# Optimization experiments

Measured on AMD Instinct MI355X. Metric: run time of the kernel, lower is better.

The kernel has to match this reference:

```python
import jax, jax.numpy as jnp
import numpy as np

N_ROUTINGS = 3


def squash(v, axis=-1):
    sn = jnp.sum(jnp.square(v), axis=axis, keepdims=True)
    return (jnp.sqrt(sn) / (1.0 + sn)) * v


def setup_inputs() -> dict:
    key = jax.random.key(0)
    k1, k2 = jax.random.split(key)
    B, R, C, n_in, d_in = 16, 14, 14, 64, 16
    n_caps, caps_dim = 10, 16
    inputs = jax.random.normal(k1, (B, R, C, n_in, d_in), dtype=jnp.float32)
    W = jax.random.normal(k2, (n_caps, n_in, d_in, caps_dim), dtype=jnp.float32) * 0.1
    return {"inputs": inputs, "W": W}


def reference(inputs, W):
    # inputs: [B,R,C,i,e], W: [n,i,e,o] -> res (u_hat): [B,R,C,n,i,o]
    res = jnp.einsum('brcie,nieo->brcnio', inputs, W)
    n_in = inputs.shape[3]
    # softmax of zeros over last axis -> uniform 1/n_in
    b = jnp.full(res.shape[:-1], 1.0 / n_in, dtype=res.dtype)  # [B,R,C,n,i]
    for _ in range(N_ROUTINGS - 1):
        v = squash(jnp.sum(b[..., None] * res, axis=-2))  # [B,R,C,n,o]
        b = b + jnp.sum(res * v[..., None, :], axis=-1)   # agreement
    out = squash(jnp.sum(b[..., None] * res, axis=-2))
    return out  # [B,R,C,n_caps,caps_dim]
```

## Files before the change

### kernel.cpp

```cpp
#include <hip/hip_runtime.h>
#include <hip/hip_bf16.h>

typedef __attribute__((ext_vector_type(4))) float f32x4;
typedef __attribute__((ext_vector_type(8))) short s16x8;

#define GLOBAL_AS __attribute__((address_space(1)))
#define LDS_AS    __attribute__((address_space(3)))
#define QPB 8


template<int CTRL>
__device__ __forceinline__ float dpp_add(float x) {
    int v = __builtin_amdgcn_update_dpp(0, __float_as_int(x), CTRL, 0xF, 0xF, true);
    return x + __int_as_float(v);
}
template<int CTRL>
__device__ __forceinline__ float dpp_movf(float x) {
    return __int_as_float(__builtin_amdgcn_update_dpp(0, __float_as_int(x), CTRL, 0xF, 0xF, true));
}

__global__ __launch_bounds__(256, 3) void caps_kernel(
    const float* __restrict__ inp,
    const float* __restrict__ W,
    float* __restrict__ out)
{
    const int tid = threadIdx.x;
    const int w   = tid >> 6;
    const int l   = tid & 63;
    const int n   = blockIdx.x / 98;
    const int qg  = blockIdx.x % 98;
    const int q0  = qg * QPB;

    extern __shared__ __align__(16) char smem[];
    char*  res_s = smem;
    float* W_s   = (float*)(smem + 16384);

    const int i4 = l >> 2;
    const int oq = l & 3;
    const int i_ = w * 16 + i4;
    const int col = l & 15;
    const int kg  = l >> 4;

    f32x4 raw[4], rawn[4];
#pragma unroll
    for (int p = 0; p < 4; ++p)
        raw[p] = *(const f32x4*)(inp + (size_t)q0 * 4096 + p * 1024 + w * 256 + l * 4);

    const float* Wn = W + (size_t)n * 16384;
    f32x4 wrot[16];
    for (int k = 0; k < 4; ++k) {
#pragma unroll
        for (int k2 = 0; k2 < 4; ++k2) {
            int d  = k2 * 256 + tid;
            int ir = d >> 6;
            int cd = d & 63;
            int c  = cd ^ (ir & 7);
            __builtin_amdgcn_global_load_lds(
                (const GLOBAL_AS unsigned int*)(Wn + (k * 1024 + ir * 64 + c) * 4),
                (LDS_AS unsigned int*)((char*)W_s + d * 16), 16, 0, 0);
        }
        __syncthreads();
        if (w == k) {
#pragma unroll
            for (int r = 0; r < 4; ++r) {
                int c = (oq + r) & 3;
#pragma unroll
                for (int kk = 0; kk < 4; ++kk) {
                    int e = c * 4 + kk;
                    wrot[r * 4 + kk] =
                        *(const f32x4*)(W_s + i4 * 256 + (((e * 4 + oq) ^ (i4 & 7)) << 2));
                }
            }
        }
        __syncthreads();
    }

    s16x8 ones;
#pragma unroll
    for (int j = 0; j < 8; ++j) ones[j] = (short)0x3F80;

#pragma unroll 2
    for (int t = 0; t < QPB; ++t) {
        const int q = q0 + t;
        char* rbuf = res_s + (t & 1) * 8192;

        if (t + 1 < QPB) {
#pragma unroll
            for (int p = 0; p < 4; ++p)
                rawn[p] = *(const f32x4*)(inp + (size_t)(q + 1) * 4096 + p * 1024 + w * 256 + l * 4);
        }

#pragma unroll
        for (int p = 0; p < 4; ++p) {
            f32x4 a = raw[p];
            f32x4 acc = (f32x4)0.0f;
#pragma unroll
            for (int kk = 0; kk < 4; ++kk) acc += a[kk] * wrot[kk];
            f32x4 b1;
#pragma unroll
            for (int kk = 0; kk < 4; ++kk) b1[kk] = dpp_movf<0x39>(a[kk]);
#pragma unroll
            for (int kk = 0; kk < 4; ++kk) acc += b1[kk] * wrot[4 + kk];
            f32x4 b2;
#pragma unroll
            for (int kk = 0; kk < 4; ++kk) b2[kk] = dpp_movf<0x4E>(a[kk]);
#pragma unroll
            for (int kk = 0; kk < 4; ++kk) acc += b2[kk] * wrot[8 + kk];
            f32x4 b3;
#pragma unroll
            for (int kk = 0; kk < 4; ++kk) b3[kk] = dpp_movf<0x93>(a[kk]);
#pragma unroll
            for (int kk = 0; kk < 4; ++kk) acc += b3[kk] * wrot[12 + kk];

#pragma unroll
            for (int dd = 0; dd < 4; ++dd) {
                int o = oq * 4 + dd;
                __hip_bfloat16 bb = __float2bfloat16(acc[dd]);
                int byte = p * 2048 + o * 128 + (((i_ >> 3) ^ (o & 7)) << 4) + (i_ & 7) * 2;
                *(unsigned short*)(rbuf + byte) = *(unsigned short*)&bb;
            }
        }

        asm volatile("s_waitcnt lgkmcnt(0)" ::: "memory");
        __builtin_amdgcn_s_barrier();
        asm volatile("" ::: "memory");
        __builtin_amdgcn_sched_barrier(0);

        s16x8 fr0 = *(const s16x8*)(rbuf + w * 2048 + col * 128 + (((kg + 0) ^ (col & 7)) << 4));
        s16x8 fr1 = *(const s16x8*)(rbuf + w * 2048 + col * 128 + (((kg + 4) ^ (col & 7)) << 4));

        f32x4 G  = (f32x4)0.0f;
        f32x4 C2 = (f32x4)0.0f;
        G  = __builtin_amdgcn_mfma_f32_16x16x32_bf16(fr0, fr0, G, 0, 0, 0);
        G  = __builtin_amdgcn_mfma_f32_16x16x32_bf16(fr1, fr1, G, 0, 0, 0);
        C2 = __builtin_amdgcn_mfma_f32_16x16x32_bf16(ones, fr0, C2, 0, 0, 0);
        C2 = __builtin_amdgcn_mfma_f32_16x16x32_bf16(ones, fr1, C2, 0, 0, 0);

        float s = C2[0] * (1.0f / 64.0f);

#pragma unroll
        for (int it = 0; it < 2; ++it) {
            float sn = s * s;
            sn = dpp_add<0xB1>(sn);
            sn = dpp_add<0x4E>(sn);
            sn = dpp_add<0x124>(sn);
            sn = dpp_add<0x128>(sn);
            float scale = sqrtf(sn) / (1.0f + sn);
            float v = scale * s;
            float v0 = __shfl(v, kg * 4 + 0);
            float v1 = __shfl(v, kg * 4 + 1);
            float v2 = __shfl(v, kg * 4 + 2);
            float v3 = __shfl(v, kg * 4 + 3);
            float acc = G[0] * v0 + G[1] * v1 + G[2] * v2 + G[3] * v3;
            acc += __shfl_xor(acc, 16);
            acc += __shfl_xor(acc, 32);
            s += acc;
        }

        float sn = s * s;
        sn = dpp_add<0xB1>(sn);
        sn = dpp_add<0x4E>(sn);
        sn = dpp_add<0x124>(sn);
        sn = dpp_add<0x128>(sn);
        float scale = sqrtf(sn) / (1.0f + sn);
        float v = scale * s;

        if (l < 16)
            out[((size_t)(q * 4 + w) * 10 + n) * 16 + col] = v;

        if (t + 1 < QPB) {
#pragma unroll
            for (int p = 0; p < 4; ++p) raw[p] = rawn[p];
        }
    }
}

extern "C" void kernel_launch(void* const* d_in, const int* in_sizes, int n_in,
                              void* d_out, int out_size, void* d_ws, size_t ws_size,
                              hipStream_t stream) {
    const float* inp = (const float*)d_in[0];
    const float* W   = (const float*)d_in[1];
    float* out = (float*)d_out;

    dim3 grid(980), block(256);
    hipLaunchKernelGGL(caps_kernel, grid, block, 32768, stream, inp, W, out);
}
```

Measured before the change: 36.39 us.

## Load W directly from global, halve positions per block, raise occupancy

After: 34.42 us. 5.4% less time.

```diff
diff --git a/kernel.cpp b/kernel.cpp
--- a/kernel.cpp
+++ b/kernel.cpp
@@ -4,9 +4,7 @@
 typedef __attribute__((ext_vector_type(4))) float f32x4;
 typedef __attribute__((ext_vector_type(8))) short s16x8;
 
-#define GLOBAL_AS __attribute__((address_space(1)))
-#define LDS_AS    __attribute__((address_space(3)))
-#define QPB 8
+#define QPB 4
 
 
 template<int CTRL>
@@ -19,7 +17,7 @@
     return __int_as_float(__builtin_amdgcn_update_dpp(0, __float_as_int(x), CTRL, 0xF, 0xF, true));
 }
 
-__global__ __launch_bounds__(256, 3) void caps_kernel(
+__global__ __launch_bounds__(256, 4) void caps_kernel(
     const float* __restrict__ inp,
     const float* __restrict__ W,
     float* __restrict__ out)
@@ -27,13 +25,12 @@
     const int tid = threadIdx.x;
     const int w   = tid >> 6;
     const int l   = tid & 63;
-    const int n   = blockIdx.x / 98;
-    const int qg  = blockIdx.x % 98;
+    const int n   = blockIdx.x / 196;
+    const int qg  = blockIdx.x % 196;
     const int q0  = qg * QPB;
 
     extern __shared__ __align__(16) char smem[];
-    char*  res_s = smem;
-    float* W_s   = (float*)(smem + 16384);
+    char* res_s = smem;
 
     const int i4 = l >> 2;
     const int oq = l & 3;
@@ -41,54 +38,28 @@
     const int col = l & 15;
     const int kg  = l >> 4;
 
-    f32x4 raw[4], rawn[4];
+    const float* wb = W + (size_t)n * 16384 + i_ * 256 + oq * 4;
+    f32x4 wrot[16];
 #pragma unroll
-    for (int p = 0; p < 4; ++p)
-        raw[p] = *(const f32x4*)(inp + (size_t)q0 * 4096 + p * 1024 + w * 256 + l * 4);
-
-    const float* Wn = W + (size_t)n * 16384;
-    f32x4 wrot[16];
-    for (int k = 0; k < 4; ++k) {
+    for (int r = 0; r < 4; ++r) {
+        int c = (oq + r) & 3;
 #pragma unroll
-        for (int k2 = 0; k2 < 4; ++k2) {
-            int d  = k2 * 256 + tid;
-            int ir = d >> 6;
-            int cd = d & 63;
-            int c  = cd ^ (ir & 7);
-            __builtin_amdgcn_global_load_lds(
-                (const GLOBAL_AS unsigned int*)(Wn + (k * 1024 + ir * 64 + c) * 4),
-                (LDS_AS unsigned int*)((char*)W_s + d * 16), 16, 0, 0);
-        }
-        __syncthreads();
-        if (w == k) {
-#pragma unroll
-            for (int r = 0; r < 4; ++r) {
-                int c = (oq + r) & 3;
-#pragma unroll
-                for (int kk = 0; kk < 4; ++kk) {
-                    int e = c * 4 + kk;
-                    wrot[r * 4 + kk] =
-                        *(const f32x4*)(W_s + i4 * 256 + (((e * 4 + oq) ^ (i4 & 7)) << 2));
-                }
-            }
-        }
-        __syncthreads();
+        for (int kk = 0; kk < 4; ++kk)
+            wrot[r * 4 + kk] = *(const f32x4*)(wb + (c * 4 + kk) * 16);
     }
 
     s16x8 ones;
 #pragma unroll
     for (int j = 0; j < 8; ++j) ones[j] = (short)0x3F80;
 
-#pragma unroll 2
     for (int t = 0; t < QPB; ++t) {
         const int q = q0 + t;
         char* rbuf = res_s + (t & 1) * 8192;
 
-        if (t + 1 < QPB) {
+        f32x4 raw[4];
 #pragma unroll
-            for (int p = 0; p < 4; ++p)
-                rawn[p] = *(const f32x4*)(inp + (size_t)(q + 1) * 4096 + p * 1024 + w * 256 + l * 4);
-        }
+        for (int p = 0; p < 4; ++p)
+            raw[p] = *(const f32x4*)(inp + (size_t)q * 4096 + p * 1024 + w * 256 + l * 4);
 
 #pragma unroll
         for (int p = 0; p < 4; ++p) {
@@ -167,11 +138,6 @@
 
         if (l < 16)
             out[((size_t)(q * 4 + w) * 10 + n) * 16 + col] = v;
-
-        if (t + 1 < QPB) {
-#pragma unroll
-            for (int p = 0; p < 4; ++p) raw[p] = rawn[p];
-        }
     }
 }
 
@@ -182,6 +148,6 @@
     const float* W   = (const float*)d_in[1];
     float* out = (float*)d_out;
 
-    dim3 grid(980), block(256);
-    hipLaunchKernelGGL(caps_kernel, grid, block, 32768, stream, inp, W, out);
+    dim3 grid(1960), block(256);
+    hipLaunchKernelGGL(caps_kernel, grid, block, 16384, stream, inp, W, out);
 }
```
